# Kernel tuning notes

Hardware: AMD Instinct MI355X
Metric: run time of the kernel (lower is better)

## Reference

```python
import jax, jax.numpy as jnp
import numpy as np

B, S, E, H = 2, 4096, 512, 8
D = E // H


def setup_inputs() -> dict:
    key = jax.random.key(0)
    ks = jax.random.split(key, 6)
    x = jax.random.normal(ks[0], (B, S, E), dtype=jnp.float32)
    scale = E ** -0.5
    in_proj_w = jax.random.normal(ks[1], (3 * E, E), dtype=jnp.float32) * scale
    in_proj_b = jnp.zeros((3 * E,), dtype=jnp.float32)
    out_proj_w = jax.random.normal(ks[2], (E, E), dtype=jnp.float32) * scale
    out_proj_b = jnp.zeros((E,), dtype=jnp.float32)
    t = jax.random.normal(ks[3], (H,), dtype=jnp.float32)
    return {"x": x, "in_proj_w": in_proj_w, "in_proj_b": in_proj_b,
            "out_proj_w": out_proj_w, "out_proj_b": out_proj_b, "t": t}


def reference(x, in_proj_w, in_proj_b, out_proj_w, out_proj_b, t):
    b, s, e = x.shape
    h, d = H, D
    # packed qkv projection as in nn.MultiheadAttention
    qkv = x @ in_proj_w.T + in_proj_b              # [b, s, 3e]
    q, k, v = jnp.split(qkv, 3, axis=-1)
    q = q.reshape(b, s, h, d).transpose(0, 2, 1, 3)  # [b, h, s, d]
    k = k.reshape(b, s, h, d).transpose(0, 2, 1, 3)
    v = v.reshape(b, s, h, d).transpose(0, 2, 1, 3)
    scores = jnp.einsum("bhqd,bhkd->bhqk", q, k) / jnp.sqrt(jnp.float32(d))
    # Gaussian relative-position bias: -(j-k)^2 / (2 * (t^2)^2), per head
    idx = jnp.arange(s)
    dist2 = (idx[None, :] - idx[:, None]).astype(jnp.float32) ** 2  # [s, s]
    sigma = t ** 2                                                  # [h]
    bias = -dist2[None, :, :] / (2.0 * (sigma ** 2)[:, None, None]) # [h, s, s]
    attn = jax.nn.softmax(scores + bias[None], axis=-1)             # [b, h, s, s]
    out = jnp.einsum("bhqk,bhkd->bhqd", attn, v)                    # [b, h, s, d]
    out = out.transpose(0, 2, 1, 3).reshape(b, s, e)
    return out @ out_proj_w.T + out_proj_b
```

## Files before the change

kernel.cpp:

```cpp
#include <hip/hip_runtime.h>
#include <hip/hip_bf16.h>
#include <stdint.h>

#define LOG2E 1.4426950408889634f

typedef __bf16 bf16;
typedef __bf16 bf16x8 __attribute__((ext_vector_type(8)));
typedef float  f32x4  __attribute__((ext_vector_type(4)));

__device__ __forceinline__ f32x4 mfma16(bf16x8 a, bf16x8 b, f32x4 c) {
    return __builtin_amdgcn_mfma_f32_16x16x32_bf16(a, b, c, 0, 0, 0);
}

__device__ __forceinline__ void async16(const void* g, void* l) {
    __builtin_amdgcn_global_load_lds(
        (const __attribute__((address_space(1))) void*)g,
        (__attribute__((address_space(3))) void*)l, 16, 0, 0);
}

__global__ __launch_bounds__(256) void qkv_gemm_kernel(
    const float* __restrict__ X, const float* __restrict__ W,
    const float* __restrict__ bias,
    bf16* __restrict__ Qb, bf16* __restrict__ Kb, bf16* __restrict__ Vt)
{
    const int tid  = threadIdx.x;
    const int lane = tid & 63;
    const int wv   = tid >> 6;
    const int quad = lane >> 4;
    const int ln   = lane & 15;
    const int bm   = blockIdx.x;
    const int bn   = blockIdx.y;

    __shared__ __align__(16) bf16 As[128 * 64];
    __shared__ __align__(16) bf16 Bs[128 * 64];

    const int wm = (wv >> 1) * 64;
    const int wn = (wv & 1) * 64;

    f32x4 acc[4][4] = {};

    for (int kt = 0; kt < 512; kt += 64) {
        #pragma unroll
        for (int i = 0; i < 4; ++i) {
            int c = tid + 256 * i;
            int row = c >> 3, cc = c & 7;
            const float* g = X + (size_t)(bm * 128 + row) * 512 + kt + cc * 8;
            float4 f0 = *(const float4*)g;
            float4 f1 = *(const float4*)(g + 4);
            bf16x8 v = { (bf16)f0.x,(bf16)f0.y,(bf16)f0.z,(bf16)f0.w,
                         (bf16)f1.x,(bf16)f1.y,(bf16)f1.z,(bf16)f1.w };
            *(bf16x8*)&As[(row * 8 + (cc ^ (row & 7))) * 8] = v;
        }
        #pragma unroll
        for (int i = 0; i < 4; ++i) {
            int c = tid + 256 * i;
            int row = c >> 3, cc = c & 7;
            const float* g = W + (size_t)(bn * 128 + row) * 512 + kt + cc * 8;
            float4 f0 = *(const float4*)g;
            float4 f1 = *(const float4*)(g + 4);
            bf16x8 v = { (bf16)f0.x,(bf16)f0.y,(bf16)f0.z,(bf16)f0.w,
                         (bf16)f1.x,(bf16)f1.y,(bf16)f1.z,(bf16)f1.w };
            *(bf16x8*)&Bs[(row * 8 + (cc ^ (row & 7))) * 8] = v;
        }
        __syncthreads();

        bf16x8 af[4][2], bfr[4][2];
        #pragma unroll
        for (int i = 0; i < 4; ++i) {
            #pragma unroll
            for (int c = 0; c < 2; ++c) {
                int ra = wm + i * 16 + ln;
                af[i][c]  = *(const bf16x8*)&As[(ra * 8 + ((c * 4 + quad) ^ (ra & 7))) * 8];
                int rb = wn + i * 16 + ln;
                bfr[i][c] = *(const bf16x8*)&Bs[(rb * 8 + ((c * 4 + quad) ^ (rb & 7))) * 8];
            }
        }
        #pragma unroll
        for (int c = 0; c < 2; ++c)
            #pragma unroll
            for (int i = 0; i < 4; ++i)
                #pragma unroll
                for (int j = 0; j < 4; ++j)
                    acc[i][j] = mfma16(af[i][c], bfr[j][c], acc[i][j]);
        __syncthreads();
    }

    #pragma unroll
    for (int i = 0; i < 4; ++i) {
        int mbase = bm * 128 + wm + i * 16 + quad * 4;
        #pragma unroll
        for (int j = 0; j < 4; ++j) {
            int n = bn * 128 + wn + j * 16 + ln;
            float bv = bias[n];
            int sec = n >> 9;
            int e = n & 511;
            int hh = e >> 6, dd = e & 63;
            #pragma unroll
            for (int r = 0; r < 4; ++r) {
                int mm = mbase + r;
                int b = mm >> 12, s = mm & 4095;
                bf16 v = (bf16)(acc[i][j][r] + bv);
                size_t bhi = (size_t)(b * 8 + hh);
                if (sec == 0)      Qb[(bhi * 4096 + s) * 64 + dd] = v;
                else if (sec == 1) Kb[(bhi * 4096 + s) * 64 + dd] = v;
                else               Vt[(bhi * 64 + dd) * 4096 + s] = v;
            }
        }
    }
}

__global__ __launch_bounds__(256) void attn_kernel(
    const bf16* __restrict__ Qb, const bf16* __restrict__ Kb,
    const bf16* __restrict__ Vt, const float* __restrict__ T,
    bf16* __restrict__ AO)
{
    const int tid  = threadIdx.x;
    const int lane = tid & 63;
    const int wv   = tid >> 6;
    const int quad = lane >> 4;
    const int ln   = lane & 15;
    const int qt   = blockIdx.x;
    const int bh   = blockIdx.y;
    const int h    = bh & 7;
    const int b    = bh >> 3;

    __shared__ __align__(16) bf16 KVs[2][2][64 * 64];
    __shared__ __align__(16) bf16 Ps[4][16 * 64];

    const float t  = T[h];
    const float s2 = t * t;
    const float cb = 1.0f / (2.0f * s2 * s2);

    const int R  = (int)ceilf(s2 * 13.4164f) + 1;
    int lo = qt * 64 - R;      if (lo < 0) lo = 0;     lo &= ~63;
    int hi = qt * 64 + 64 + R; if (hi > 4096) hi = 4096; hi = (hi + 63) & ~63;

    const float c1  = 0.125f * LOG2E;
    const float c2m = -cb * LOG2E;
    const float c3m = -12.0f * LOG2E;

    const int qrow_f = qt * 64 + wv * 16 + ln;
    const bf16* qptr = Qb + ((size_t)bh * 4096 + qrow_f) * 64 + quad * 8;
    bf16x8 qf0 = *(const bf16x8*)qptr;
    bf16x8 qf1 = *(const bf16x8*)(qptr + 32);

    const int qrow_c = qt * 64 + wv * 16 + quad * 4;
    const float fln = (float)ln;

    f32x4 o[4] = {};
    f32x4 lsum = {};
    const bf16 one = (bf16)1.0f;
    const bf16x8 onesv = { one, one, one, one, one, one, one, one };

    const int srow = tid >> 3;
    const int scc  = tid & 7;

    for (int ct = lo; ct < hi; ct += 128) {
        const int ntiles = ((hi - ct) >= 128) ? 2 : 1;
        __syncthreads();
        #pragma unroll
        for (int tt = 0; tt < 2; ++tt) {
            if (tt < ntiles) {
                const bf16* Kg = Kb + ((size_t)bh * 4096 + ct + tt * 64) * 64;
                const bf16* Vg = Vt + (size_t)bh * 64 * 4096 + ct + tt * 64;
                bf16* Ksl = &KVs[tt][0][0];
                bf16* Vsl = &KVs[tt][1][0];
                #pragma unroll
                for (int i = 0; i < 2; ++i) {
                    int c = tid + 256 * i;
                    int row = srow + 32 * i;
                    int cg = scc ^ (row & 7);
                    async16(Kg + row * 64 + cg * 8, Ksl + c * 8);
                    async16(Vg + (size_t)row * 4096 + cg * 8, Vsl + c * 8);
                }
            }
        }
        __syncthreads();

        for (int tt = 0; tt < ntiles; ++tt) {
            const int kt = ct + tt * 64;
            const bf16* Ks = &KVs[tt][0][0];
            const bf16* Vs = &KVs[tt][1][0];

            f32x4 sc[4] = {};
            #pragma unroll
            for (int tI = 0; tI < 4; ++tI) {
                int row = tI * 16 + ln;
                bf16x8 kf0 = *(const bf16x8*)&Ks[(row * 8 + ((quad    ) ^ (row & 7))) * 8];
                bf16x8 kf1 = *(const bf16x8*)&Ks[(row * 8 + ((4 + quad) ^ (row & 7))) * 8];
                sc[tI] = mfma16(qf0, kf0, sc[tI]);
                sc[tI] = mfma16(qf1, kf1, sc[tI]);
            }

            float p[4][4];
            #pragma unroll
            for (int r = 0; r < 4; ++r) {
                float Ar = (float)(qrow_c + r - kt) - fln;
                #pragma unroll
                for (int tI = 0; tI < 4; ++tI) {
                    float df = Ar - (float)(tI * 16);
                    float lg = fmaf(sc[tI][r], c1, fmaf(df, df * c2m, c3m));
                    p[tI][r] = __builtin_amdgcn_exp2f(lg);
                }
            }

            #pragma unroll
            for (int tI = 0; tI < 4; ++tI)
                #pragma unroll
                for (int r = 0; r < 4; ++r) {
                    int row = quad * 4 + r;
                    int cc  = tI * 2 + (ln >> 3);
                    int idx = row * 64 + ((cc ^ (row & 7)) * 8) + (ln & 7);
                    Ps[wv][idx] = (bf16)p[tI][r];
                }

            bf16x8 pf[2];
            #pragma unroll
            for (int c = 0; c < 2; ++c)
                pf[c] = *(const bf16x8*)&Ps[wv][(ln * 8 + ((c * 4 + quad) ^ (ln & 7))) * 8];

            #pragma unroll
            for (int c = 0; c < 2; ++c)
                lsum = mfma16(pf[c], onesv, lsum);
            #pragma unroll
            for (int t2 = 0; t2 < 4; ++t2) {
                int vrow = t2 * 16 + ln;
                #pragma unroll
                for (int c = 0; c < 2; ++c) {
                    bf16x8 vf = *(const bf16x8*)&Vs[(vrow * 8 + ((c * 4 + quad) ^ (vrow & 7))) * 8];
                    o[t2] = mfma16(pf[c], vf, o[t2]);
                }
            }
        }
    }

    float il[4];
    #pragma unroll
    for (int r = 0; r < 4; ++r) il[r] = __builtin_amdgcn_rcpf(lsum[r]);
    #pragma unroll
    for (int t2 = 0; t2 < 4; ++t2) {
        int dd = t2 * 16 + ln;
        #pragma unroll
        for (int r = 0; r < 4; ++r) {
            int s = qt * 64 + wv * 16 + quad * 4 + r;
            AO[((size_t)(b * 4096 + s)) * 512 + h * 64 + dd] = (bf16)(o[t2][r] * il[r]);
        }
    }
}

__global__ __launch_bounds__(256) void out_gemm_kernel(
    const bf16* __restrict__ A, const float* __restrict__ W,
    const float* __restrict__ bias, float* __restrict__ OUT)
{
    const int tid  = threadIdx.x;
    const int lane = tid & 63;
    const int wv   = tid >> 6;
    const int quad = lane >> 4;
    const int ln   = lane & 15;
    const int bm   = blockIdx.x;
    const int bn   = blockIdx.y;

    __shared__ __align__(16) bf16 As[128 * 64];
    __shared__ __align__(16) bf16 Bs[128 * 64];

    const int wm = (wv >> 1) * 64;
    const int wn = (wv & 1) * 64;

    f32x4 acc[4][4] = {};

    for (int kt = 0; kt < 512; kt += 64) {
        #pragma unroll
        for (int i = 0; i < 4; ++i) {
            int c = tid + 256 * i;
            int row = c >> 3, cc = c & 7;
            uint4 v = *(const uint4*)&A[(size_t)(bm * 128 + row) * 512 + kt + cc * 8];
            *(uint4*)&As[(row * 8 + (cc ^ (row & 7))) * 8] = v;
        }
        #pragma unroll
        for (int i = 0; i < 4; ++i) {
            int c = tid + 256 * i;
            int row = c >> 3, cc = c & 7;
            const float* g = W + (size_t)(bn * 128 + row) * 512 + kt + cc * 8;
            float4 f0 = *(const float4*)g;
            float4 f1 = *(const float4*)(g + 4);
            bf16x8 v = { (bf16)f0.x,(bf16)f0.y,(bf16)f0.z,(bf16)f0.w,
                         (bf16)f1.x,(bf16)f1.y,(bf16)f1.z,(bf16)f1.w };
            *(bf16x8*)&Bs[(row * 8 + (cc ^ (row & 7))) * 8] = v;
        }
        __syncthreads();

        bf16x8 af[4][2], bfr[4][2];
        #pragma unroll
        for (int i = 0; i < 4; ++i) {
            #pragma unroll
            for (int c = 0; c < 2; ++c) {
                int ra = wm + i * 16 + ln;
                af[i][c]  = *(const bf16x8*)&As[(ra * 8 + ((c * 4 + quad) ^ (ra & 7))) * 8];
                int rb = wn + i * 16 + ln;
                bfr[i][c] = *(const bf16x8*)&Bs[(rb * 8 + ((c * 4 + quad) ^ (rb & 7))) * 8];
            }
        }
        #pragma unroll
        for (int c = 0; c < 2; ++c)
            #pragma unroll
            for (int i = 0; i < 4; ++i)
                #pragma unroll
                for (int j = 0; j < 4; ++j)
                    acc[i][j] = mfma16(af[i][c], bfr[j][c], acc[i][j]);
        __syncthreads();
    }

    #pragma unroll
    for (int i = 0; i < 4; ++i) {
        int mbase = bm * 128 + wm + i * 16 + quad * 4;
        #pragma unroll
        for (int j = 0; j < 4; ++j) {
            int n = bn * 128 + wn + j * 16 + ln;
            float bv = bias[n];
            #pragma unroll
            for (int r = 0; r < 4; ++r)
                OUT[(size_t)(mbase + r) * 512 + n] = acc[i][j][r] + bv;
        }
    }
}

extern "C" void kernel_launch(void* const* d_in, const int* in_sizes, int n_in,
                              void* d_out, int out_size, void* d_ws, size_t ws_size,
                              hipStream_t stream)
{
    const float* x  = (const float*)d_in[0];
    const float* wi = (const float*)d_in[1];
    const float* bi = (const float*)d_in[2];
    const float* wo = (const float*)d_in[3];
    const float* bo = (const float*)d_in[4];
    const float* t  = (const float*)d_in[5];
    float* out = (float*)d_out;

    bf16* Qb = (bf16*)d_ws;
    bf16* Kb = Qb + 4194304;
    bf16* Vt = Kb + 4194304;
    bf16* AO = Vt + 4194304;

    qkv_gemm_kernel<<<dim3(64, 12), 256, 0, stream>>>(x, wi, bi, Qb, Kb, Vt);
    attn_kernel   <<<dim3(64, 16), 256, 0, stream>>>(Qb, Kb, Vt, t, AO);
    out_gemm_kernel<<<dim3(64, 4), 256, 0, stream>>>(AO, wo, bo, out);
}
```

Before: 139.0 us.

## Pre-convert inputs to bf16 and stage GEMM tiles via async global-to-LDS loads

Adds a conversion kernel that casts X, the input projection weights and the output projection weights to bf16 in workspace once per call. Both GEMM kernels then load bf16 tiles straight into LDS with global_load_lds, with the XOR swizzle moved onto the source address. This removes the repeated fp32 loads and in-register conversions from the GEMM main loops, including reconverting each weight tile across many blocks. The cost is an extra kernel launch plus an extra read and write pass over X, and more workspace.

```diff
diff --git a/kernel.cpp b/kernel.cpp
--- a/kernel.cpp
+++ b/kernel.cpp
@@ -18,8 +18,25 @@
         (__attribute__((address_space(3))) void*)l, 16, 0, 0);
 }
 
+__global__ __launch_bounds__(256) void cvt_kernel(
+    const float* __restrict__ X, const float* __restrict__ Wi,
+    const float* __restrict__ Wo,
+    bf16* __restrict__ Xb, bf16* __restrict__ Wib, bf16* __restrict__ Wob)
+{
+    size_t e = ((size_t)blockIdx.x * 256 + threadIdx.x) * 8;
+    const float* src; bf16* dst; size_t off;
+    if (e < 4194304)      { src = X;  dst = Xb;  off = e; }
+    else if (e < 4980736) { src = Wi; dst = Wib; off = e - 4194304; }
+    else                  { src = Wo; dst = Wob; off = e - 4980736; }
+    float4 f0 = *(const float4*)(src + off);
+    float4 f1 = *(const float4*)(src + off + 4);
+    bf16x8 v = { (bf16)f0.x,(bf16)f0.y,(bf16)f0.z,(bf16)f0.w,
+                 (bf16)f1.x,(bf16)f1.y,(bf16)f1.z,(bf16)f1.w };
+    *(bf16x8*)(dst + off) = v;
+}
+
 __global__ __launch_bounds__(256) void qkv_gemm_kernel(
-    const float* __restrict__ X, const float* __restrict__ W,
+    const bf16* __restrict__ Xb, const bf16* __restrict__ Wb,
     const float* __restrict__ bias,
     bf16* __restrict__ Qb, bf16* __restrict__ Kb, bf16* __restrict__ Vt)
 {
@@ -37,30 +54,22 @@
     const int wm = (wv >> 1) * 64;
     const int wn = (wv & 1) * 64;
 
+    const int srow = tid >> 3;
+    const int scc  = tid & 7;
+
+    const bf16* XA = Xb + (size_t)bm * 128 * 512;
+    const bf16* WB = Wb + (size_t)bn * 128 * 512;
+
     f32x4 acc[4][4] = {};
 
     for (int kt = 0; kt < 512; kt += 64) {
         #pragma unroll
         for (int i = 0; i < 4; ++i) {
-            int c = tid + 256 * i;
-            int row = c >> 3, cc = c & 7;
-            const float* g = X + (size_t)(bm * 128 + row) * 512 + kt + cc * 8;
-            float4 f0 = *(const float4*)g;
-            float4 f1 = *(const float4*)(g + 4);
-            bf16x8 v = { (bf16)f0.x,(bf16)f0.y,(bf16)f0.z,(bf16)f0.w,
-                         (bf16)f1.x,(bf16)f1.y,(bf16)f1.z,(bf16)f1.w };
-            *(bf16x8*)&As[(row * 8 + (cc ^ (row & 7))) * 8] = v;
-        }
-        #pragma unroll
-        for (int i = 0; i < 4; ++i) {
-            int c = tid + 256 * i;
-            int row = c >> 3, cc = c & 7;
-            const float* g = W + (size_t)(bn * 128 + row) * 512 + kt + cc * 8;
-            float4 f0 = *(const float4*)g;
-            float4 f1 = *(const float4*)(g + 4);
-            bf16x8 v = { (bf16)f0.x,(bf16)f0.y,(bf16)f0.z,(bf16)f0.w,
-                         (bf16)f1.x,(bf16)f1.y,(bf16)f1.z,(bf16)f1.w };
-            *(bf16x8*)&Bs[(row * 8 + (cc ^ (row & 7))) * 8] = v;
+            int c   = tid + 256 * i;
+            int row = srow + 32 * i;
+            int cg  = scc ^ (row & 7);
+            async16(XA + (size_t)row * 512 + kt + cg * 8, As + c * 8);
+            async16(WB + (size_t)row * 512 + kt + cg * 8, Bs + c * 8);
         }
         __syncthreads();
 
@@ -249,7 +258,7 @@
 }
 
 __global__ __launch_bounds__(256) void out_gemm_kernel(
-    const bf16* __restrict__ A, const float* __restrict__ W,
+    const bf16* __restrict__ A, const bf16* __restrict__ Wb,
     const float* __restrict__ bias, float* __restrict__ OUT)
 {
     const int tid  = threadIdx.x;
@@ -266,26 +275,22 @@
     const int wm = (wv >> 1) * 64;
     const int wn = (wv & 1) * 64;
 
+    const int srow = tid >> 3;
+    const int scc  = tid & 7;
+
+    const bf16* AA = A  + (size_t)bm * 128 * 512;
+    const bf16* WB = Wb + (size_t)bn * 128 * 512;
+
     f32x4 acc[4][4] = {};
 
     for (int kt = 0; kt < 512; kt += 64) {
         #pragma unroll
         for (int i = 0; i < 4; ++i) {
-            int c = tid + 256 * i;
-            int row = c >> 3, cc = c & 7;
-            uint4 v = *(const uint4*)&A[(size_t)(bm * 128 + row) * 512 + kt + cc * 8];
-            *(uint4*)&As[(row * 8 + (cc ^ (row & 7))) * 8] = v;
-        }
-        #pragma unroll
-        for (int i = 0; i < 4; ++i) {
-            int c = tid + 256 * i;
-            int row = c >> 3, cc = c & 7;
-            const float* g = W + (size_t)(bn * 128 + row) * 512 + kt + cc * 8;
-            float4 f0 = *(const float4*)g;
-            float4 f1 = *(const float4*)(g + 4);
-            bf16x8 v = { (bf16)f0.x,(bf16)f0.y,(bf16)f0.z,(bf16)f0.w,
-                         (bf16)f1.x,(bf16)f1.y,(bf16)f1.z,(bf16)f1.w };
-            *(bf16x8*)&Bs[(row * 8 + (cc ^ (row & 7))) * 8] = v;
+            int c   = tid + 256 * i;
+            int row = srow + 32 * i;
+            int cg  = scc ^ (row & 7);
+            async16(AA + (size_t)row * 512 + kt + cg * 8, As + c * 8);
+            async16(WB + (size_t)row * 512 + kt + cg * 8, Bs + c * 8);
         }
         __syncthreads();
 
@@ -336,12 +341,16 @@
     const float* t  = (const float*)d_in[5];
     float* out = (float*)d_out;
 
-    bf16* Qb = (bf16*)d_ws;
-    bf16* Kb = Qb + 4194304;
-    bf16* Vt = Kb + 4194304;
-    bf16* AO = Vt + 4194304;
-
-    qkv_gemm_kernel<<<dim3(64, 12), 256, 0, stream>>>(x, wi, bi, Qb, Kb, Vt);
-    attn_kernel   <<<dim3(64, 16), 256, 0, stream>>>(Qb, Kb, Vt, t, AO);
-    out_gemm_kernel<<<dim3(64, 4), 256, 0, stream>>>(AO, wo, bo, out);
-}
+    bf16* Qb  = (bf16*)d_ws;
+    bf16* Kb  = Qb  + 4194304;
+    bf16* Vt  = Kb  + 4194304;
+    bf16* AO  = Vt  + 4194304;
+    bf16* Xb  = AO  + 4194304;
+    bf16* Wib = Xb  + 4194304;
+    bf16* Wob = Wib + 786432;
+
+    cvt_kernel     <<<dim3(2560), 256, 0, stream>>>(x, wi, wo, Xb, Wib, Wob);
+    qkv_gemm_kernel<<<dim3(64, 12), 256, 0, stream>>>(Xb, Wib, bi, Qb, Kb, Vt);
+    attn_kernel    <<<dim3(64, 16), 256, 0, stream>>>(Qb, Kb, Vt, t, AO);
+    out_gemm_kernel<<<dim3(64, 4), 256, 0, stream>>>(AO, Wob, bo, out);
+}
```

Measured after the change: 128.5 us. -7.6%, faster.
